# Optimization experiments

Measured on AMD Instinct MI355X. Metric: run time of the kernel, lower is better.

## Reference

```python
import jax, jax.numpy as jnp
import numpy as np

DIM = 128
WH, WW = 8, 8
N = WH * WW            # tokens per window = 64
H = 8                  # num_heads
HD = DIM // H          # head_dim = 16
SCALE = HD ** -0.5
B = 2                  # true batch
NW = 1024              # windows per image (256x256 / 8x8)
B_ = B * NW            # 2048 windows total
NFT = 2                # num_frame_type
TABLE = (2 * WH - 1) * (2 * WW - 1)  # 225


def _relative_position_index():
    coords = np.stack(np.meshgrid(np.arange(WH), np.arange(WW), indexing='ij'))  # (2, WH, WW)
    cf = coords.reshape(2, -1)                        # (2, N)
    rel = cf[:, :, None] - cf[:, None, :]             # (2, N, N)
    rel = rel.transpose(1, 2, 0).astype(np.int64)     # (N, N, 2)
    rel[..., 0] += WH - 1
    rel[..., 1] += WW - 1
    rel[..., 0] *= 2 * WW - 1
    return rel.sum(-1)                                # (N, N) in [0, 224]


def setup_inputs() -> dict:
    key = jax.random.key(0)
    ks = jax.random.split(key, 12)
    x = jax.random.normal(ks[0], (B_, N, DIM), dtype=jnp.float32)
    # 0 / -100 additive window mask (shifted-window pattern surrogate)
    mask = jnp.where(jax.random.uniform(ks[1], (NW, N, N)) > 0.9, -100.0, 0.0).astype(jnp.float32)
    frame_type = jax.random.uniform(ks[2], (B, NFT), dtype=jnp.float32)
    qkv_w = jax.random.normal(ks[3], (3 * DIM, DIM), dtype=jnp.float32) * 0.02
    qkv_b = jnp.zeros((3 * DIM,), dtype=jnp.float32)
    table = jax.random.normal(ks[4], (TABLE, H), dtype=jnp.float32) * 0.02
    proj_w = jax.random.normal(ks[5], (DIM, DIM), dtype=jnp.float32) * 0.02
    proj_b = jnp.zeros((DIM,), dtype=jnp.float32)
    aff_w1 = jax.random.normal(ks[6], (16, NFT), dtype=jnp.float32) * 0.1
    aff_b1 = jnp.zeros((16,), dtype=jnp.float32)
    aff_w2 = jax.random.normal(ks[7], (2 * DIM, 16), dtype=jnp.float32) * 0.1
    rel_index = jnp.asarray(_relative_position_index(), dtype=jnp.int32)
    return {"x": x, "mask": mask, "frame_type": frame_type,
            "qkv_w": qkv_w, "qkv_b": qkv_b, "table": table,
            "proj_w": proj_w, "proj_b": proj_b,
            "aff_w1": aff_w1, "aff_b1": aff_b1, "aff_w2": aff_w2,
            "rel_index": rel_index}


def reference(x, mask, frame_type, qkv_w, qkv_b, table, proj_w, proj_b,
              aff_w1, aff_b1, aff_w2, rel_index):
    # qkv projection: (B_, N, 3C) -> (3, B_, H, N, HD)
    qkv = (x @ qkv_w.T + qkv_b).reshape(B_, N, 3, H, HD).transpose(2, 0, 3, 1, 4)
    q, k, v = qkv[0], qkv[1], qkv[2]
    attn = jnp.einsum('bhnd,bhmd->bhnm', q * SCALE, k)          # (B_, H, N, N)
    rpb = table[rel_index].transpose(2, 0, 1)                    # (H, N, N)
    attn = attn + rpb[None]
    # add window mask: (B, NW, H, N, N)
    attn = attn.reshape(B_ // NW, NW, H, N, N) + mask[None, :, None]
    attn = jax.nn.softmax(attn.reshape(B_, H, N, N), axis=-1)
    # FA affine modulation of V
    hdn = jax.nn.sigmoid(frame_type @ aff_w1.T + aff_b1)         # (B, 16)
    ap = hdn @ aff_w2.T                                          # (B, 2C)
    scale_p, bias_p = jnp.split(ap, 2, axis=-1)                  # each (B, C)
    scale_p = jnp.repeat(scale_p, B_ // B, axis=0).reshape(B_, H, 1, HD)
    bias_p = jnp.repeat(bias_p, B_ // B, axis=0).reshape(B_, H, 1, HD)
    v = jax.nn.softplus(scale_p) * v + bias_p
    out = jnp.einsum('bhnm,bhmd->bhnd', attn, v)                 # (B_, H, N, HD)
    out = out.transpose(0, 2, 1, 3).reshape(B_, N, DIM)
    return out @ proj_w.T + proj_b
```

## Files before the change

kernel.cpp:

```cpp
#include <hip/hip_runtime.h>
#include <hip/hip_bf16.h>

#define NWIN 2048
#define LOG2E 1.44269504f
#define QSCALE 0.36067376f

#define OFF_AFF 0
#define OFF_RPB 512
#define OFF_WQ  33280
#define OFF_WP  57856

typedef __attribute__((ext_vector_type(8))) __bf16 bf16x8;
typedef __attribute__((ext_vector_type(4))) float floatx4;
typedef __attribute__((ext_vector_type(4))) short short4v;

#if __has_builtin(__builtin_amdgcn_exp2f)
#define EXP2F __builtin_amdgcn_exp2f
#else
#define EXP2F exp2f
#endif

__global__ __launch_bounds__(256) void prep_kernel(
    const float* __restrict__ frame_type, const float* __restrict__ qkv_w,
    const float* __restrict__ table, const float* __restrict__ proj_w,
    const float* __restrict__ aff_w1, const float* __restrict__ aff_b1,
    const float* __restrict__ aff_w2, const int* __restrict__ rel_index,
    float* __restrict__ ws)
{
  const int gid = blockIdx.x * 256 + threadIdx.x;
  if (gid < 49152) {
    int j = gid & 7, lane = (gid >> 3) & 63, kt = (gid >> 9) & 3, nt = gid >> 11;
    int n = nt * 16 + (lane & 15);
    int k = kt * 32 + (lane >> 4) * 8 + j;
    ((__bf16*)(ws + OFF_WQ))[gid] = (__bf16)qkv_w[n * 128 + k];
  }
  if (gid < 16384) {
    int j = gid & 3, lane = (gid >> 2) & 63, nt = (gid >> 8) & 7, h = gid >> 11;
    int n = nt * 16 + (lane & 15);
    int k = h * 16 + (lane >> 4) * 4 + j;
    ((__bf16*)(ws + OFF_WP))[gid] = (__bf16)proj_w[n * 128 + k];
  }
  if (gid < 32768) {
    int h = gid >> 12, rem = gid & 4095, row = rem >> 6, col = rem & 63;
    int dst = h * 4096 + row * 64 + (col & 15) * 4 + (col >> 4);
    ws[OFF_RPB + dst] = table[rel_index[rem] * 8 + h] * LOG2E;
  }
  if (gid < 512) {
    int b = gid >> 8, c2 = gid & 255;
    float hd[16];
    #pragma unroll
    for (int j = 0; j < 16; ++j) {
      float t = frame_type[b*2+0]*aff_w1[j*2+0] + frame_type[b*2+1]*aff_w1[j*2+1] + aff_b1[j];
      hd[j] = 1.0f / (1.0f + expf(-t));
    }
    float ap = 0.f;
    #pragma unroll
    for (int j = 0; j < 16; ++j) ap += hd[j] * aff_w2[c2*16 + j];
    float r = (c2 < 128) ? ((ap > 20.f) ? ap : log1pf(expf(ap))) : ap;
    ws[OFF_AFF + gid] = r;
  }
}

__global__ __launch_bounds__(256, 3) void attn_kernel(
    const float* __restrict__ x, const float* __restrict__ mask,
    const float* __restrict__ qkv_b, const float* __restrict__ proj_b,
    const float* __restrict__ ws, float* __restrict__ out)
{
  __shared__ __attribute__((aligned(16))) __bf16 sQP[64 * 136];
  __shared__ __attribute__((aligned(16))) __bf16 sK [64 * 136];
  __shared__ __attribute__((aligned(16))) __bf16 sVT[128 * 72];

  const int w    = blockIdx.x;
  const int b    = w >> 10;
  const int tid  = threadIdx.x;
  const int wv   = tid >> 6;
  const int lane = tid & 63;
  const int quad = lane >> 4;
  const int l15  = lane & 15;
  const int row0 = wv * 16;

  bf16x8 af[4][4];
  {
    const float* xw = x + (size_t)w * 8192;
    #pragma unroll
    for (int mt = 0; mt < 4; ++mt)
      #pragma unroll
      for (int kt = 0; kt < 4; ++kt) {
        const float* p = xw + (mt*16 + l15) * 128 + kt*32 + quad*8;
        float4 f0 = *(const float4*)p;
        float4 f1 = *(const float4*)(p + 4);
        bf16x8 v;
        v[0]=(__bf16)f0.x; v[1]=(__bf16)f0.y; v[2]=(__bf16)f0.z; v[3]=(__bf16)f0.w;
        v[4]=(__bf16)f1.x; v[5]=(__bf16)f1.y; v[6]=(__bf16)f1.z; v[7]=(__bf16)f1.w;
        af[mt][kt] = v;
      }
  }

  {
    const __bf16* wq = (const __bf16*)(ws + OFF_WQ);
    for (int t = 0; t < 6; ++t) {
      const int nt = wv + t * 4;
      bf16x8 bfr[4];
      #pragma unroll
      for (int kt = 0; kt < 4; ++kt)
        bfr[kt] = *(const bf16x8*)(wq + ((size_t)(nt*4 + kt) * 64 + lane) * 8);
      const float bias = qkv_b[nt*16 + l15];
      const int col = nt*16 + l15;
      #pragma unroll
      for (int mt = 0; mt < 4; ++mt) {
        floatx4 acc = {bias, bias, bias, bias};
        #pragma unroll
        for (int kt = 0; kt < 4; ++kt)
          acc = __builtin_amdgcn_mfma_f32_16x16x32_bf16(af[mt][kt], bfr[kt], acc, 0, 0, 0);
        const int rowb = mt*16 + quad*4;
        if (nt < 8) {
          #pragma unroll
          for (int r = 0; r < 4; ++r) sQP[(rowb + r)*136 + col] = (__bf16)(acc[r] * QSCALE);
        } else if (nt < 16) {
          const int c = col - 128;
          #pragma unroll
          for (int r = 0; r < 4; ++r) sK[(rowb + r)*136 + c] = (__bf16)acc[r];
        } else {
          const int c = col - 256;
          const float sp = ws[OFF_AFF + b*256 + c];
          const float bp = ws[OFF_AFF + b*256 + 128 + c];
          #pragma unroll
          for (int r = 0; r < 4; ++r) sVT[c*72 + rowb + r] = (__bf16)fmaf(sp, acc[r], bp);
        }
      }
    }
  }
  __syncthreads();

  short4v qa[8];
  #pragma unroll
  for (int h = 0; h < 8; ++h)
    qa[h] = *(const short4v*)(&sQP[(row0 + l15)*136 + h*16 + quad*4]);

  __bf16* sP = sQP + wv * 2176;

  float mv[4][4];
  {
    const float* mrow = mask + (size_t)(w & 1023) * 4096;
    #pragma unroll
    for (int jt = 0; jt < 4; ++jt)
      #pragma unroll
      for (int r = 0; r < 4; ++r)
        mv[jt][r] = mrow[(row0 + quad*4 + r)*64 + jt*16 + l15] * LOG2E;
  }
  floatx4 pacc[8];
  #pragma unroll
  for (int nt = 0; nt < 8; ++nt) {
    float pb = proj_b[nt*16 + l15];
    pacc[nt] = (floatx4){pb, pb, pb, pb};
  }

  bf16x8 ones;
  #pragma unroll
  for (int i = 0; i < 8; ++i) ones[i] = (__bf16)1.0f;

  const float* rpb = ws + OFF_RPB;
  const __bf16* wp = (const __bf16*)(ws + OFF_WP);

  #pragma unroll 1
  for (int h = 0; h < 8; ++h) {
    floatx4 rq[4];
    #pragma unroll
    for (int r = 0; r < 4; ++r)
      rq[r] = *(const floatx4*)(rpb + h*4096 + (row0 + quad*4 + r)*64 + l15*4);
    short4v wpf[8];
    #pragma unroll
    for (int nt = 0; nt < 8; ++nt)
      wpf[nt] = *(const short4v*)(wp + ((size_t)(h*8 + nt)*64 + lane)*4);

    short4v kb[4];
    #pragma unroll
    for (int jt = 0; jt < 4; ++jt)
      kb[jt] = *(const short4v*)(&sK[(jt*16 + l15)*136 + h*16 + quad*4]);

    floatx4 s[4];
    #pragma unroll
    for (int jt = 0; jt < 4; ++jt) {
      floatx4 ci;
      #pragma unroll
      for (int r = 0; r < 4; ++r) ci[r] = rq[r][jt] + mv[jt][r];
      s[jt] = __builtin_amdgcn_mfma_f32_16x16x16bf16_1k(qa[h], kb[jt], ci, 0, 0, 0);
    }
    #pragma unroll
    for (int jt = 0; jt < 4; ++jt)
      #pragma unroll
      for (int r = 0; r < 4; ++r)
        sP[(quad*4 + r)*72 + jt*16 + l15] = (__bf16)EXP2F(s[jt][r]);

    floatx4 o2 = {0.f,0.f,0.f,0.f}, s2 = {0.f,0.f,0.f,0.f};
    #pragma unroll
    for (int kt = 0; kt < 2; ++kt) {
      bf16x8 pa = *(const bf16x8*)(&sP[l15*72 + kt*32 + quad*8]);
      bf16x8 vb = *(const bf16x8*)(&sVT[(h*16 + l15)*72 + kt*32 + quad*8]);
      o2 = __builtin_amdgcn_mfma_f32_16x16x32_bf16(vb, pa, o2, 0, 0, 0);
      s2 = __builtin_amdgcn_mfma_f32_16x16x32_bf16(ones, pa, s2, 0, 0, 0);
    }
    const float inv = 1.0f / s2[0];
    union { short4v s; __bf16 hh[4]; } u;
    #pragma unroll
    for (int r = 0; r < 4; ++r) u.hh[r] = (__bf16)(o2[r] * inv);
    #pragma unroll
    for (int nt = 0; nt < 8; ++nt)
      pacc[nt] = __builtin_amdgcn_mfma_f32_16x16x16bf16_1k(u.s, wpf[nt], pacc[nt], 0, 0, 0);
  }

  {
    float* ow = out + (size_t)w * 8192;
    #pragma unroll
    for (int nt = 0; nt < 8; ++nt)
      #pragma unroll
      for (int r = 0; r < 4; ++r)
        ow[(row0 + quad*4 + r)*128 + nt*16 + l15] = pacc[nt][r];
  }
}

extern "C" void kernel_launch(void* const* d_in, const int* in_sizes, int n_in,
                              void* d_out, int out_size, void* d_ws, size_t ws_size,
                              hipStream_t stream)
{
  const float* x          = (const float*)d_in[0];
  const float* mask       = (const float*)d_in[1];
  const float* frame_type = (const float*)d_in[2];
  const float* qkv_w      = (const float*)d_in[3];
  const float* qkv_b      = (const float*)d_in[4];
  const float* table      = (const float*)d_in[5];
  const float* proj_w     = (const float*)d_in[6];
  const float* proj_b     = (const float*)d_in[7];
  const float* aff_w1     = (const float*)d_in[8];
  const float* aff_b1     = (const float*)d_in[9];
  const float* aff_w2     = (const float*)d_in[10];
  const int*   rel_index  = (const int*)d_in[11];
  float* ws   = (float*)d_ws;
  float* outp = (float*)d_out;

  prep_kernel<<<192, 256, 0, stream>>>(frame_type, qkv_w, table, proj_w,
                                       aff_w1, aff_b1, aff_w2, rel_index, ws);
  attn_kernel<<<NWIN, 256, 0, stream>>>(x, mask, qkv_b, proj_b, ws, outp);
}
```

Baseline: 219.6 us.

## Restructure QKV projection per-wave with transposed MFMA and XOR-swizzled LDS layouts

Each wave now projects only its own 16 tokens, with x as the B operand, so the Q fragments stay in registers and the Q staging buffer in LDS goes away. K, V^T and P are stored in unpadded LDS arrays with XOR swizzles to avoid bank conflicts, which shrinks shared memory. Occupancy hint rises from 3 to 4 blocks per CU. The wave's QKV loop is fully unrolled with weight loads inline, and proj weight loads are moved into the MFMA loop. This may raise register pressure and change load latency hiding.

Result: slower. 242.2 us (+10.3%).

```diff
diff --git a/kernel.cpp b/kernel.cpp
--- a/kernel.cpp
+++ b/kernel.cpp
@@ -29,8 +29,8 @@
 {
   const int gid = blockIdx.x * 256 + threadIdx.x;
   if (gid < 49152) {
-    int j = gid & 7, lane = (gid >> 3) & 63, kt = (gid >> 9) & 3, nt = gid >> 11;
-    int n = nt * 16 + (lane & 15);
+    int j = gid & 7, lane = (gid >> 3) & 63, kt = (gid >> 9) & 3, t = gid >> 11;
+    int n = t * 16 + (lane & 15);
     int k = kt * 32 + (lane >> 4) * 8 + j;
     ((__bf16*)(ws + OFF_WQ))[gid] = (__bf16)qkv_w[n * 128 + k];
   }
@@ -61,14 +61,14 @@
   }
 }
 
-__global__ __launch_bounds__(256, 3) void attn_kernel(
+__global__ __launch_bounds__(256, 4) void attn_kernel(
     const float* __restrict__ x, const float* __restrict__ mask,
     const float* __restrict__ qkv_b, const float* __restrict__ proj_b,
     const float* __restrict__ ws, float* __restrict__ out)
 {
-  __shared__ __attribute__((aligned(16))) __bf16 sQP[64 * 136];
-  __shared__ __attribute__((aligned(16))) __bf16 sK [64 * 136];
-  __shared__ __attribute__((aligned(16))) __bf16 sVT[128 * 72];
+  __shared__ __attribute__((aligned(16))) __bf16 sK [64 * 128];
+  __shared__ __attribute__((aligned(16))) __bf16 sVT[128 * 64];
+  __shared__ __attribute__((aligned(16))) __bf16 sP [4 * 16 * 64];
 
   const int w    = blockIdx.x;
   const int b    = w >> 10;
@@ -78,66 +78,69 @@
   const int quad = lane >> 4;
   const int l15  = lane & 15;
   const int row0 = wv * 16;
-
-  bf16x8 af[4][4];
+  const int token = row0 + l15;
+
+  bf16x8 xf[4];
   {
-    const float* xw = x + (size_t)w * 8192;
-    #pragma unroll
-    for (int mt = 0; mt < 4; ++mt)
-      #pragma unroll
-      for (int kt = 0; kt < 4; ++kt) {
-        const float* p = xw + (mt*16 + l15) * 128 + kt*32 + quad*8;
-        float4 f0 = *(const float4*)p;
-        float4 f1 = *(const float4*)(p + 4);
-        bf16x8 v;
-        v[0]=(__bf16)f0.x; v[1]=(__bf16)f0.y; v[2]=(__bf16)f0.z; v[3]=(__bf16)f0.w;
-        v[4]=(__bf16)f1.x; v[5]=(__bf16)f1.y; v[6]=(__bf16)f1.z; v[7]=(__bf16)f1.w;
-        af[mt][kt] = v;
-      }
-  }
-
-  {
-    const __bf16* wq = (const __bf16*)(ws + OFF_WQ);
-    for (int t = 0; t < 6; ++t) {
-      const int nt = wv + t * 4;
-      bf16x8 bfr[4];
-      #pragma unroll
-      for (int kt = 0; kt < 4; ++kt)
-        bfr[kt] = *(const bf16x8*)(wq + ((size_t)(nt*4 + kt) * 64 + lane) * 8);
-      const float bias = qkv_b[nt*16 + l15];
-      const int col = nt*16 + l15;
-      #pragma unroll
-      for (int mt = 0; mt < 4; ++mt) {
-        floatx4 acc = {bias, bias, bias, bias};
-        #pragma unroll
-        for (int kt = 0; kt < 4; ++kt)
-          acc = __builtin_amdgcn_mfma_f32_16x16x32_bf16(af[mt][kt], bfr[kt], acc, 0, 0, 0);
-        const int rowb = mt*16 + quad*4;
-        if (nt < 8) {
-          #pragma unroll
-          for (int r = 0; r < 4; ++r) sQP[(rowb + r)*136 + col] = (__bf16)(acc[r] * QSCALE);
-        } else if (nt < 16) {
-          const int c = col - 128;
-          #pragma unroll
-          for (int r = 0; r < 4; ++r) sK[(rowb + r)*136 + c] = (__bf16)acc[r];
-        } else {
-          const int c = col - 256;
-          const float sp = ws[OFF_AFF + b*256 + c];
-          const float bp = ws[OFF_AFF + b*256 + 128 + c];
-          #pragma unroll
-          for (int r = 0; r < 4; ++r) sVT[c*72 + rowb + r] = (__bf16)fmaf(sp, acc[r], bp);
-        }
-      }
+    const float* xw = x + (size_t)w * 8192 + (size_t)token * 128;
+    #pragma unroll
+    for (int kt = 0; kt < 4; ++kt) {
+      const float* p = xw + kt*32 + quad*8;
+      float4 f0 = *(const float4*)p;
+      float4 f1 = *(const float4*)(p + 4);
+      bf16x8 v;
+      v[0]=(__bf16)f0.x; v[1]=(__bf16)f0.y; v[2]=(__bf16)f0.z; v[3]=(__bf16)f0.w;
+      v[4]=(__bf16)f1.x; v[5]=(__bf16)f1.y; v[6]=(__bf16)f1.z; v[7]=(__bf16)f1.w;
+      xf[kt] = v;
+    }
+  }
+
+  const __bf16* wq = (const __bf16*)(ws + OFF_WQ);
+  short4v qa[8];
+
+  #pragma unroll
+  for (int t = 0; t < 8; ++t) {
+    floatx4 acc = *(const floatx4*)(qkv_b + t*16 + quad*4);
+    #pragma unroll
+    for (int kt = 0; kt < 4; ++kt)
+      acc = __builtin_amdgcn_mfma_f32_16x16x32_bf16(
+          *(const bf16x8*)(wq + ((size_t)(t*4 + kt) * 64 + lane) * 8), xf[kt], acc, 0, 0, 0);
+    union { short4v s; __bf16 hh[4]; } u;
+    #pragma unroll
+    for (int r = 0; r < 4; ++r) u.hh[r] = (__bf16)(acc[r] * QSCALE);
+    qa[t] = u.s;
+  }
+  #pragma unroll
+  for (int t = 8; t < 16; ++t) {
+    floatx4 acc = *(const floatx4*)(qkv_b + t*16 + quad*4);
+    #pragma unroll
+    for (int kt = 0; kt < 4; ++kt)
+      acc = __builtin_amdgcn_mfma_f32_16x16x32_bf16(
+          *(const bf16x8*)(wq + ((size_t)(t*4 + kt) * 64 + lane) * 8), xf[kt], acc, 0, 0, 0);
+    const int dblk = (t - 8) * 4 + quad;
+    const int sw = (dblk ^ (token & 31)) * 4;
+    #pragma unroll
+    for (int r = 0; r < 4; ++r)
+      sK[token * 128 + sw + r] = (__bf16)acc[r];
+  }
+  #pragma unroll
+  for (int t = 16; t < 24; ++t) {
+    floatx4 acc = *(const floatx4*)(qkv_b + t*16 + quad*4);
+    #pragma unroll
+    for (int kt = 0; kt < 4; ++kt)
+      acc = __builtin_amdgcn_mfma_f32_16x16x32_bf16(
+          *(const bf16x8*)(wq + ((size_t)(t*4 + kt) * 64 + lane) * 8), xf[kt], acc, 0, 0, 0);
+    const int c0 = (t - 16) * 16 + quad * 4;
+    floatx4 sp = *(const floatx4*)(ws + OFF_AFF + b*256 + c0);
+    floatx4 bp = *(const floatx4*)(ws + OFF_AFF + b*256 + 128 + c0);
+    #pragma unroll
+    for (int r = 0; r < 4; ++r) {
+      const int c = c0 + r;
+      const int blk = ((token >> 3) ^ (c & 7)) * 8;
+      sVT[c * 64 + blk + (token & 7)] = (__bf16)fmaf(sp[r], acc[r], bp[r]);
     }
   }
   __syncthreads();
-
-  short4v qa[8];
-  #pragma unroll
-  for (int h = 0; h < 8; ++h)
-    qa[h] = *(const short4v*)(&sQP[(row0 + l15)*136 + h*16 + quad*4]);
-
-  __bf16* sP = sQP + wv * 2176;
 
   float mv[4][4];
   {
@@ -161,6 +164,7 @@
 
   const float* rpb = ws + OFF_RPB;
   const __bf16* wp = (const __bf16*)(ws + OFF_WP);
+  __bf16* sPw = sP + wv * 1024;
 
   #pragma unroll 1
   for (int h = 0; h < 8; ++h) {
@@ -168,35 +172,32 @@
     #pragma unroll
     for (int r = 0; r < 4; ++r)
       rq[r] = *(const floatx4*)(rpb + h*4096 + (row0 + quad*4 + r)*64 + l15*4);
-    short4v wpf[8];
-    #pragma unroll
-    for (int nt = 0; nt < 8; ++nt)
-      wpf[nt] = *(const short4v*)(wp + ((size_t)(h*8 + nt)*64 + lane)*4);
-
-    short4v kb[4];
-    #pragma unroll
-    for (int jt = 0; jt < 4; ++jt)
-      kb[jt] = *(const short4v*)(&sK[(jt*16 + l15)*136 + h*16 + quad*4]);
 
     floatx4 s[4];
     #pragma unroll
     for (int jt = 0; jt < 4; ++jt) {
+      const int tj = jt*16 + l15;
+      short4v kb = *(const short4v*)(&sK[tj * 128 + ((h*4 + quad) ^ (tj & 31)) * 4]);
       floatx4 ci;
       #pragma unroll
       for (int r = 0; r < 4; ++r) ci[r] = rq[r][jt] + mv[jt][r];
-      s[jt] = __builtin_amdgcn_mfma_f32_16x16x16bf16_1k(qa[h], kb[jt], ci, 0, 0, 0);
-    }
-    #pragma unroll
-    for (int jt = 0; jt < 4; ++jt)
-      #pragma unroll
-      for (int r = 0; r < 4; ++r)
-        sP[(quad*4 + r)*72 + jt*16 + l15] = (__bf16)EXP2F(s[jt][r]);
-
+      s[jt] = __builtin_amdgcn_mfma_f32_16x16x16bf16_1k(qa[h], kb, ci, 0, 0, 0);
+    }
+    #pragma unroll
+    for (int jt = 0; jt < 4; ++jt) {
+      const int cb = jt*2 + (l15 >> 3);
+      #pragma unroll
+      for (int r = 0; r < 4; ++r) {
+        const int rl = quad*4 + r;
+        sPw[rl*64 + ((cb ^ (rl & 7)) * 8) + (l15 & 7)] = (__bf16)EXP2F(s[jt][r]);
+      }
+    }
     floatx4 o2 = {0.f,0.f,0.f,0.f}, s2 = {0.f,0.f,0.f,0.f};
     #pragma unroll
     for (int kt = 0; kt < 2; ++kt) {
-      bf16x8 pa = *(const bf16x8*)(&sP[l15*72 + kt*32 + quad*8]);
-      bf16x8 vb = *(const bf16x8*)(&sVT[(h*16 + l15)*72 + kt*32 + quad*8]);
+      const int blk = ((kt*4 + quad) ^ (l15 & 7)) * 8;
+      bf16x8 pa = *(const bf16x8*)(&sPw[l15*64 + blk]);
+      bf16x8 vb = *(const bf16x8*)(&sVT[(h*16 + l15)*64 + blk]);
       o2 = __builtin_amdgcn_mfma_f32_16x16x32_bf16(vb, pa, o2, 0, 0, 0);
       s2 = __builtin_amdgcn_mfma_f32_16x16x32_bf16(ones, pa, s2, 0, 0, 0);
     }
@@ -205,8 +206,10 @@
     #pragma unroll
     for (int r = 0; r < 4; ++r) u.hh[r] = (__bf16)(o2[r] * inv);
     #pragma unroll
-    for (int nt = 0; nt < 8; ++nt)
-      pacc[nt] = __builtin_amdgcn_mfma_f32_16x16x16bf16_1k(u.s, wpf[nt], pacc[nt], 0, 0, 0);
+    for (int nt = 0; nt < 8; ++nt) {
+      short4v wpf = *(const short4v*)(wp + ((size_t)(h*8 + nt)*64 + lane)*4);
+      pacc[nt] = __builtin_amdgcn_mfma_f32_16x16x16bf16_1k(u.s, wpf, pacc[nt], 0, 0, 0);
+    }
   }
 
   {
```
